# Optimization experiments

Hardware: AMD Instinct MI355X
Metric: run time of the kernel (lower is better)

The kernel has to match this reference:

```python
import jax, jax.numpy as jnp
import numpy as np

N = 8192
IN_DIM = 256
OUT_DIM = 256


def setup_inputs() -> dict:
    key = jax.random.key(0)
    k1, k2, k3, k4 = jax.random.split(key, 4)
    x = jax.random.normal(k1, (N, IN_DIM), dtype=jnp.float32)
    adj = jax.random.uniform(k2, (N, N), dtype=jnp.float32)
    # nn.Linear(in_dim, out_dim): weight [out,in], bias [out]. Store W as [in,out].
    bound = 1.0 / np.sqrt(IN_DIM)
    W = jax.random.uniform(k3, (IN_DIM, OUT_DIM), dtype=jnp.float32, minval=-bound, maxval=bound)
    b = jax.random.uniform(k4, (OUT_DIM,), dtype=jnp.float32, minval=-bound, maxval=bound)
    return {"x": x, "adj": adj, "W": W, "b": b}


def reference(x, adj, W, b):
    # ReLU( D^{-1/2} (A + I) D^{-1/2} X W + b )
    # A_hat = adj + I; degree = A_hat.sum(axis=1)
    n = adj.shape[0]
    A_hat = adj + jnp.eye(n, dtype=adj.dtype)
    degree = A_hat.sum(axis=1)
    d_inv_sqrt = degree ** -0.5  # [N]
    # D^{-1/2} @ A_hat @ D^{-1/2} == row-scale then col-scale (no NxN diag matmuls)
    A_norm = A_hat * d_inv_sqrt[:, None] * d_inv_sqrt[None, :]
    out = A_norm @ x          # [N, in_dim]
    out = out @ W + b         # [N, out_dim]
    return jax.nn.relu(out)
```

## Files before the change

kernel.cpp:

```cpp
#include <hip/hip_runtime.h>
#include <hip/hip_bf16.h>


typedef __attribute__((ext_vector_type(8))) short short8;
typedef __attribute__((ext_vector_type(4))) short short4v;
typedef __attribute__((ext_vector_type(4))) float floatx4;

#define GLDS16(g, l) __builtin_amdgcn_global_load_lds(\
    (const __attribute__((address_space(1))) void*)(g), \
    (__attribute__((address_space(3))) void*)(l), 16, 0, 0)

__device__ __forceinline__ unsigned short f2b(float f) {
  unsigned int x = __builtin_bit_cast(unsigned int, f);
  unsigned int r = (x + 0x7fffu + ((x >> 16) & 1u)) >> 16;
  return (unsigned short)r;
}

__global__ __launch_bounds__(256) void k_prep(
    const float* __restrict__ adj, const float* __restrict__ W,
    const float* __restrict__ X, float* __restrict__ s,
    unsigned short* __restrict__ WT, unsigned short* __restrict__ Xb) {
  __shared__ float part[4];
  const int b = blockIdx.x, t = threadIdx.x;
  if (b < 8192) {
    const float4* row = (const float4*)(adj + (size_t)b * 8192);
    float sum = 0.f;
#pragma unroll
    for (int q = 0; q < 8; ++q) {
      float4 v = row[t + q * 256];
      sum += v.x + v.y + v.z + v.w;
    }
#pragma unroll
    for (int o = 32; o > 0; o >>= 1) sum += __shfl_down(sum, o, 64);
    if ((t & 63) == 0) part[t >> 6] = sum;
    __syncthreads();
    if (t == 0) s[b] = rsqrtf(part[0] + part[1] + part[2] + part[3] + 1.0f);
  } else if (b < 8256) {
    const int wb = b - 8192;
#pragma unroll
    for (int q = 0; q < 4; ++q) {
      int i = wb * 1024 + q * 256 + t;
      WT[i] = f2b(W[(i & 255) * 256 + (i >> 8)]);
    }
  } else {
    const int xb = b - 8256;
#pragma unroll
    for (int q = 0; q < 8; ++q) {
      int i = xb * 2048 + q * 256 + t;
      Xb[i] = f2b(X[i]);
    }
  }
}

__global__ __launch_bounds__(256) void k_xw(
    const unsigned short* __restrict__ Xb, const unsigned short* __restrict__ WT,
    const float* __restrict__ bias, const float* __restrict__ s,
    float* __restrict__ Zd, unsigned short* __restrict__ ZsT) {
  __shared__ __align__(16) unsigned short ldsX[64 * 256];
  __shared__ __align__(16) unsigned short ldsW[64 * 256];
  const int t = threadIdx.x, l = t & 63, w = t >> 6;
  const int quad = l >> 4, nl = l & 15;
  const int m0 = blockIdx.x * 64, n0 = blockIdx.y * 64;
#pragma unroll
  for (int r = 0; r < 8; ++r) {
    int sl = r * 256 + t;
    int kc = sl >> 6, mm = sl & 63;
    GLDS16(Xb + (m0 + mm) * 256 + kc * 8, (char*)ldsX + sl * 16);
    GLDS16(WT + (n0 + mm) * 256 + kc * 8, (char*)ldsW + sl * 16);
  }
  __syncthreads();
  const int wm = w & 1, wn = w >> 1;
  floatx4 acc[2][2] = {};
#pragma unroll
  for (int kk = 0; kk < 8; ++kk) {
    int kc = kk * 4 + quad;
    short8 af[2], bf[2];
#pragma unroll
    for (int i = 0; i < 2; ++i) {
      af[i] = *(const short8*)&ldsX[(kc * 64 + wm * 32 + i * 16 + nl) * 8];
      bf[i] = *(const short8*)&ldsW[(kc * 64 + wn * 32 + i * 16 + nl) * 8];
    }
#pragma unroll
    for (int mi = 0; mi < 2; ++mi)
#pragma unroll
      for (int ni = 0; ni < 2; ++ni)
        acc[mi][ni] = __builtin_amdgcn_mfma_f32_16x16x32_bf16(af[mi], bf[ni], acc[mi][ni], 0, 0, 0);
  }
#pragma unroll
  for (int mi = 0; mi < 2; ++mi)
#pragma unroll
    for (int ni = 0; ni < 2; ++ni)
#pragma unroll
      for (int r = 0; r < 4; ++r) {
        int row = m0 + wm * 32 + mi * 16 + quad * 4 + r;
        int col = n0 + wn * 32 + ni * 16 + nl;
        float v = acc[mi][ni][r];
        float sr = s[row];
        Zd[row * 256 + col] = sr * sr * v + bias[col];
        ZsT[col * 8192 + row] = f2b(sr * v);
      }
}

__global__ __launch_bounds__(512) void k_main(
    const float* __restrict__ adj, const unsigned short* __restrict__ ZsT,
    const float* __restrict__ s, const float* __restrict__ Zd,
    float* __restrict__ out) {
  __shared__ __align__(16) char ldsA[8 * 544];
  __shared__ __align__(16) unsigned short ldsB[64 * 256];
  const int t = threadIdx.x, l = t & 63, w = t >> 6;
  const int quad = l >> 4, nl = l & 15;
  const int m0 = blockIdx.x * 32;
  const int aM = t >> 4, aC = t & 15;
  const float* aSrc = adj + (size_t)(m0 + aM) * 8192 + aC * 4;
  char* aDst = ldsA + (aC >> 1) * 544 + aM * 16 + (aC & 1) * 8;
  floatx4 acc[2][2] = {};
  for (int kt = 0; kt < 128; ++kt) {
    const int k0 = kt * 64;
    __syncthreads();
#pragma unroll
    for (int r = 0; r < 4; ++r) {
      int sl = r * 512 + t;
      GLDS16(ZsT + (sl & 255) * 8192 + k0 + (sl >> 8) * 8, (char*)ldsB + sl * 16);
    }
    float4 av = *(const float4*)(aSrc + k0);
    short4v ab = { (short)f2b(av.x), (short)f2b(av.y), (short)f2b(av.z), (short)f2b(av.w) };
    *(short4v*)aDst = ab;
    __syncthreads();
#pragma unroll
    for (int kk = 0; kk < 2; ++kk) {
      int kc = kk * 4 + quad;
      short8 af[2], bf[2];
      af[0] = *(const short8*)(ldsA + kc * 544 + nl * 16);
      af[1] = *(const short8*)(ldsA + kc * 544 + (16 + nl) * 16);
      bf[0] = *(const short8*)&ldsB[(kc * 256 + w * 32 + nl) * 8];
      bf[1] = *(const short8*)&ldsB[(kc * 256 + w * 32 + 16 + nl) * 8];
      acc[0][0] = __builtin_amdgcn_mfma_f32_16x16x32_bf16(af[0], bf[0], acc[0][0], 0, 0, 0);
      acc[0][1] = __builtin_amdgcn_mfma_f32_16x16x32_bf16(af[0], bf[1], acc[0][1], 0, 0, 0);
      acc[1][0] = __builtin_amdgcn_mfma_f32_16x16x32_bf16(af[1], bf[0], acc[1][0], 0, 0, 0);
      acc[1][1] = __builtin_amdgcn_mfma_f32_16x16x32_bf16(af[1], bf[1], acc[1][1], 0, 0, 0);
    }
  }
#pragma unroll
  for (int mi = 0; mi < 2; ++mi)
#pragma unroll
    for (int ni = 0; ni < 2; ++ni)
#pragma unroll
      for (int r = 0; r < 4; ++r) {
        int row = m0 + mi * 16 + quad * 4 + r;
        int col = w * 32 + ni * 16 + nl;
        float v = s[row] * acc[mi][ni][r] + Zd[row * 256 + col];
        out[row * 256 + col] = v > 0.f ? v : 0.f;
      }
}

extern "C" void kernel_launch(void* const* d_in, const int* in_sizes, int n_in,
                              void* d_out, int out_size, void* d_ws, size_t ws_size,
                              hipStream_t stream) {
  const float* X    = (const float*)d_in[0];
  const float* adj  = (const float*)d_in[1];
  const float* W    = (const float*)d_in[2];
  const float* bias = (const float*)d_in[3];
  float* out = (float*)d_out;

  char* ws = (char*)d_ws;
  float* s            = (float*)(ws);
  unsigned short* WT  = (unsigned short*)(ws + 32768);
  unsigned short* Xb  = (unsigned short*)(ws + 262144);
  float* Zd           = (float*)(ws + (8 << 20));
  unsigned short* ZsT = (unsigned short*)(ws + (16 << 20));

  hipLaunchKernelGGL(k_prep, dim3(9280), dim3(256), 0, stream, adj, W, X, s, WT, Xb);
  hipLaunchKernelGGL(k_xw, dim3(128, 4), dim3(256), 0, stream, Xb, WT, bias, s, Zd, ZsT);
  hipLaunchKernelGGL(k_main, dim3(256), dim3(512), 0, stream, adj, ZsT, s, Zd, out);
}
```

Measured before the change: 621.5 us.

## Double-buffer main GEMM tiles and pre-block Z into contiguous k-tiles

The main aggregation kernel now double-buffers both the adjacency tile and the Z tile in LDS. It prefetches the next k-tile's global loads while MFMAs run on the current one, which leaves one barrier per iteration instead of two. The XW kernel now stages its scaled bf16 output through LDS and writes it in a k-tile-blocked layout, so each main-kernel tile load reads one contiguous 32KB chunk rather than strided rows. This costs twice the LDS, which may reduce occupancy, plus an extra LDS staging step in k_xw.

```diff
diff --git a/kernel.cpp b/kernel.cpp
--- a/kernel.cpp
+++ b/kernel.cpp
@@ -55,9 +55,10 @@
 __global__ __launch_bounds__(256) void k_xw(
     const unsigned short* __restrict__ Xb, const unsigned short* __restrict__ WT,
     const float* __restrict__ bias, const float* __restrict__ s,
-    float* __restrict__ Zd, unsigned short* __restrict__ ZsT) {
+    float* __restrict__ Zd, unsigned short* __restrict__ Zsb) {
   __shared__ __align__(16) unsigned short ldsX[64 * 256];
   __shared__ __align__(16) unsigned short ldsW[64 * 256];
+  __shared__ __align__(16) unsigned short ldsT[64 * 72];
   const int t = threadIdx.x, l = t & 63, w = t >> 6;
   const int quad = l >> 4, nl = l & 15;
   const int m0 = blockIdx.x * 64, n0 = blockIdx.y * 64;
@@ -97,49 +98,73 @@
         float v = acc[mi][ni][r];
         float sr = s[row];
         Zd[row * 256 + col] = sr * sr * v + bias[col];
-        ZsT[col * 8192 + row] = f2b(sr * v);
+        ldsT[(col - n0) * 72 + (row - m0)] = f2b(sr * v);
       }
+  __syncthreads();
+#pragma unroll
+  for (int h = 0; h < 2; ++h) {
+    int c = h * 256 + t;
+    int kc = c >> 6, nn = c & 63;
+    short8 val = *(const short8*)&ldsT[nn * 72 + kc * 8];
+    *(short8*)(Zsb + (size_t)blockIdx.x * 16384 + kc * 2048 + (n0 + nn) * 8) = val;
+  }
 }
 
 __global__ __launch_bounds__(512) void k_main(
-    const float* __restrict__ adj, const unsigned short* __restrict__ ZsT,
+    const float* __restrict__ adj, const unsigned short* __restrict__ Zsb,
     const float* __restrict__ s, const float* __restrict__ Zd,
     float* __restrict__ out) {
-  __shared__ __align__(16) char ldsA[8 * 544];
-  __shared__ __align__(16) unsigned short ldsB[64 * 256];
+  __shared__ __align__(16) char ldsA[2][8 * 544];
+  __shared__ __align__(16) unsigned short ldsB[2][64 * 256];
   const int t = threadIdx.x, l = t & 63, w = t >> 6;
   const int quad = l >> 4, nl = l & 15;
   const int m0 = blockIdx.x * 32;
   const int aM = t >> 4, aC = t & 15;
   const float* aSrc = adj + (size_t)(m0 + aM) * 8192 + aC * 4;
-  char* aDst = ldsA + (aC >> 1) * 544 + aM * 16 + (aC & 1) * 8;
+  const int aOff = (aC >> 1) * 544 + aM * 16 + (aC & 1) * 8;
   floatx4 acc[2][2] = {};
+
+  float4 av = *(const float4*)(aSrc);
+#pragma unroll
+  for (int r = 0; r < 4; ++r) {
+    int sl = r * 512 + t;
+    GLDS16(Zsb + (size_t)sl * 8, (char*)ldsB[0] + sl * 16);
+  }
+  {
+    short4v ab = {(short)f2b(av.x), (short)f2b(av.y), (short)f2b(av.z), (short)f2b(av.w)};
+    *(short4v*)(ldsA[0] + aOff) = ab;
+  }
+  __syncthreads();
+
   for (int kt = 0; kt < 128; ++kt) {
-    const int k0 = kt * 64;
-    __syncthreads();
+    const int cur = kt & 1, nxt = cur ^ 1;
+    const int ktn = (kt < 127) ? kt + 1 : 127;
+    av = *(const float4*)(aSrc + (size_t)ktn * 64);
 #pragma unroll
     for (int r = 0; r < 4; ++r) {
       int sl = r * 512 + t;
-      GLDS16(ZsT + (sl & 255) * 8192 + k0 + (sl >> 8) * 8, (char*)ldsB + sl * 16);
-    }
-    float4 av = *(const float4*)(aSrc + k0);
-    short4v ab = { (short)f2b(av.x), (short)f2b(av.y), (short)f2b(av.z), (short)f2b(av.w) };
-    *(short4v*)aDst = ab;
-    __syncthreads();
+      GLDS16(Zsb + (size_t)(ktn * 2048 + sl) * 8, (char*)ldsB[nxt] + sl * 16);
+    }
 #pragma unroll
     for (int kk = 0; kk < 2; ++kk) {
       int kc = kk * 4 + quad;
       short8 af[2], bf[2];
-      af[0] = *(const short8*)(ldsA + kc * 544 + nl * 16);
-      af[1] = *(const short8*)(ldsA + kc * 544 + (16 + nl) * 16);
-      bf[0] = *(const short8*)&ldsB[(kc * 256 + w * 32 + nl) * 8];
-      bf[1] = *(const short8*)&ldsB[(kc * 256 + w * 32 + 16 + nl) * 8];
+      af[0] = *(const short8*)(ldsA[cur] + kc * 544 + nl * 16);
+      af[1] = *(const short8*)(ldsA[cur] + kc * 544 + (16 + nl) * 16);
+      bf[0] = *(const short8*)&ldsB[cur][(kc * 256 + w * 32 + nl) * 8];
+      bf[1] = *(const short8*)&ldsB[cur][(kc * 256 + w * 32 + 16 + nl) * 8];
       acc[0][0] = __builtin_amdgcn_mfma_f32_16x16x32_bf16(af[0], bf[0], acc[0][0], 0, 0, 0);
       acc[0][1] = __builtin_amdgcn_mfma_f32_16x16x32_bf16(af[0], bf[1], acc[0][1], 0, 0, 0);
       acc[1][0] = __builtin_amdgcn_mfma_f32_16x16x32_bf16(af[1], bf[0], acc[1][0], 0, 0, 0);
       acc[1][1] = __builtin_amdgcn_mfma_f32_16x16x32_bf16(af[1], bf[1], acc[1][1], 0, 0, 0);
     }
-  }
+    {
+      short4v ab = {(short)f2b(av.x), (short)f2b(av.y), (short)f2b(av.z), (short)f2b(av.w)};
+      *(short4v*)(ldsA[nxt] + aOff) = ab;
+    }
+    __syncthreads();
+  }
+
 #pragma unroll
   for (int mi = 0; mi < 2; ++mi)
 #pragma unroll
@@ -167,9 +192,9 @@
   unsigned short* WT  = (unsigned short*)(ws + 32768);
   unsigned short* Xb  = (unsigned short*)(ws + 262144);
   float* Zd           = (float*)(ws + (8 << 20));
-  unsigned short* ZsT = (unsigned short*)(ws + (16 << 20));
+  unsigned short* Zsb = (unsigned short*)(ws + (16 << 20));
 
   hipLaunchKernelGGL(k_prep, dim3(9280), dim3(256), 0, stream, adj, W, X, s, WT, Xb);
-  hipLaunchKernelGGL(k_xw, dim3(128, 4), dim3(256), 0, stream, Xb, WT, bias, s, Zd, ZsT);
-  hipLaunchKernelGGL(k_main, dim3(256), dim3(512), 0, stream, adj, ZsT, s, Zd, out);
-}
+  hipLaunchKernelGGL(k_xw, dim3(128, 4), dim3(256), 0, stream, Xb, WT, bias, s, Zd, Zsb);
+  hipLaunchKernelGGL(k_main, dim3(256), dim3(512), 0, stream, adj, Zsb, s, Zd, out);
+}
```

Measured after the change: 528.6 us. -15.0%, faster.
